# Performance work log

Hardware: AMD Instinct MI355X
Metric: run time of the kernel (lower is better)

Reference implementation:

```python
import jax, jax.numpy as jnp
import numpy as np

D = 16        # d_model
DFF = 128     # ffn hidden
H_NN = 128    # pairwise-MLP hidden
RES = 1.0     # res_ratio (undefined global in source; standard residual)
EPS = 1e-6


def setup_inputs() -> dict:
    key = jax.random.key(0)
    ks = jax.random.split(key, 16)
    B, G, L = 8, 1, 256
    def n(k, shape, s=0.05):
        return jax.random.normal(k, shape, jnp.float32) * s
    return dict(
        x=jax.random.normal(ks[0], (B, G, L, D), jnp.float32),
        mask=jnp.zeros((B, G, L, L), jnp.float32),
        wq=n(ks[1], (D, D)), bq=jnp.zeros((D,), jnp.float32),
        wk=n(ks[2], (D, D)), bk=jnp.zeros((D,), jnp.float32),
        wv=n(ks[3], (D, D)), bv=jnp.zeros((D,), jnp.float32),
        wo=n(ks[4], (D, D)), bo=jnp.zeros((D,), jnp.float32),
        nn_w1=n(ks[5], (2 * D, H_NN)), nn_b1=jnp.zeros((H_NN,), jnp.float32),
        nn_w2=n(ks[6], (H_NN, 1)), nn_b2=jnp.zeros((1,), jnp.float32),
        f1=n(ks[7], (D, DFF)), f1b=jnp.zeros((DFF,), jnp.float32),
        f2=n(ks[8], (DFF, D)), f2b=jnp.zeros((D,), jnp.float32),
        g1=jnp.ones((D,), jnp.float32), be1=jnp.zeros((D,), jnp.float32),
        g2=jnp.ones((D,), jnp.float32), be2=jnp.zeros((D,), jnp.float32),
    )


def _layernorm(x, g, b):
    m = jnp.mean(x, -1, keepdims=True)
    v = jnp.var(x, -1, keepdims=True)
    return (x - m) * jax.lax.rsqrt(v + EPS) * g + b


def reference(x, mask, wq, bq, wk, bk, wv, bv, wo, bo,
              nn_w1, nn_b1, nn_w2, nn_b2,
              f1, f1b, f2, f2b, g1, be1, g2, be2):
    # projections: (B,G,L,D)
    q = x @ wq + bq
    k = x @ wk + bk
    v = x @ wv + bv
    # pairwise relation-network attention.
    # NN(concat([q_i, k_j])) first layer splits as q_i @ W1[:D] + k_j @ W1[D:]
    w1q, w1k = nn_w1[:D], nn_w1[D:]
    w2 = nn_w2[:, 0]
    qa = q @ w1q  # (B,G,L,H)
    kb = k @ w1k
    h1 = jax.nn.relu(qa[:, :, :, None, :] + kb[:, :, None, :, :] + nn_b1)  # (B,G,Lq,Lk,H)
    logits = jnp.einsum('bgijh,h->bgij', h1, w2) + nn_b2[0]
    # make_sym: NN(concat([k_j, q_i])) -> k_j @ W1[:D] + q_i @ W1[D:]
    ka = k @ w1q
    qb = q @ w1k
    h2 = jax.nn.relu(qb[:, :, :, None, :] + ka[:, :, None, :, :] + nn_b1)
    logits = logits + jnp.einsum('bgijh,h->bgij', h2, w2) + nn_b2[0]
    logits = logits + mask * -1e9
    attn = jax.nn.softmax(logits, axis=-1)          # (B,G,Lq,Lk)
    ctx = jnp.einsum('bgij,bgjd->bgid', attn, v)    # (B,G,L,D)
    attn_out = ctx @ wo + bo
    out1 = _layernorm(RES * x + (2.0 - RES) * attn_out, g1, be1)
    ffn = jax.nn.relu(out1 @ f1 + f1b) @ f2 + f2b
    out2 = _layernorm(RES * out1 + (2.0 - RES) * ffn, g2, be2)
    return out2
```

## Files before the change

kernel.cpp:

```cpp
#include <hip/hip_runtime.h>
#include <hip/hip_bf16.h>

typedef __hip_bfloat16 bf16;
typedef float f32x4 __attribute__((ext_vector_type(4)));

constexpr int DIM  = 16;
constexpr int HNN  = 128;
constexpr int SEQ  = 256;
constexpr int BAT  = 8;
constexpr int ROWS = BAT * SEQ;
constexpr int HP   = HNN / 2;
constexpr int QT   = 4;
constexpr int NQT  = ROWS / QT;
constexpr int QHP  = 16;

__device__ __forceinline__ bool is_f32(const void* g1) {
  return ((const unsigned*)g1)[0] == 0x3F800000u;
}
__device__ __forceinline__ float ld(const void* p, long i, bool f32) {
  return f32 ? ((const float*)p)[i]
             : __bfloat162float(((const bf16*)p)[i]);
}

__global__ __launch_bounds__(128) void prep_kernel(
    const void* __restrict__ x,
    const void* __restrict__ wq, const void* __restrict__ bq,
    const void* __restrict__ wk, const void* __restrict__ bk,
    const void* __restrict__ wv, const void* __restrict__ bv,
    const void* __restrict__ nn_w1, const void* __restrict__ nn_b1,
    const void* __restrict__ nn_w2, const void* __restrict__ g1flag,
    float* __restrict__ kkT, float* __restrict__ qq,
    float* __restrict__ vT,  float2* __restrict__ w2p)
{
  const bool f32 = is_f32(g1flag);
  const int row = blockIdx.x;
  const int tid = threadIdx.x;
  __shared__ float xs[DIM], qs[DIM], ks[DIM], vs[DIM];

  if (tid < DIM) xs[tid] = ld(x, (long)row * DIM + tid, f32);
  __syncthreads();

  if (tid < 3 * DIM) {
    const int which = tid >> 4, d = tid & 15;
    const void* w  = (which == 0) ? wq : (which == 1) ? wk : wv;
    const void* bb = (which == 0) ? bq : (which == 1) ? bk : bv;
    float acc = ld(bb, d, f32);
    #pragma unroll
    for (int e = 0; e < DIM; e++) acc += xs[e] * ld(w, e * DIM + d, f32);
    if (which == 0) qs[d] = acc;
    else if (which == 1) ks[d] = acc;
    else vs[d] = acc;
  }
  __syncthreads();

  float qw1q = 0.f, qw1k = 0.f, kw1q = 0.f, kw1k = 0.f;
  #pragma unroll
  for (int d = 0; d < DIM; d++) {
    float a = ld(nn_w1, d * HNN + tid, f32);
    float b = ld(nn_w1, (DIM + d) * HNN + tid, f32);
    qw1q += qs[d] * a;  qw1k += qs[d] * b;
    kw1q += ks[d] * a;  kw1k += ks[d] * b;
  }
  const float b1 = ld(nn_b1, tid, f32);
  const int hp = tid >> 1, half = tid & 1;
  ((float2*)kkT)[((size_t)hp * ROWS + row) * 2 + half] =
      make_float2(kw1k + b1, kw1q + b1);
  ((float2*)qq)[((size_t)row * HP + hp) * 2 + half] =
      make_float2(qw1q, qw1k);
  if (tid < DIM) vT[tid * ROWS + row] = vs[tid];
  if (row == 0 && tid < HP)
    w2p[tid] = make_float2(ld(nn_w2, 2 * tid, f32), ld(nn_w2, 2 * tid + 1, f32));
}

__global__ __launch_bounds__(256) void logits_kernel(
    const f32x4* __restrict__ kkT, const f32x4* __restrict__ qq,
    const float2* __restrict__ w2p, float* __restrict__ part)
{
  const int bid     = blockIdx.x;
  const int qt      = bid & (NQT - 1);
  const int quarter = bid >> 9;
  const int bi = qt >> 6;
  const int i0 = (qt & 63) * QT;
  const int j  = threadIdx.x;
  const int col = bi * SEQ + j;

  const f32x4* kkbase = kkT + (size_t)quarter * QHP * ROWS + col;
  const f32x4* qbase  = qq + (size_t)(bi * SEQ + i0) * HP + quarter * QHP;
  const float2* wbase = w2p + quarter * QHP;

  const f32x4 z = {0.f, 0.f, 0.f, 0.f};
  f32x4 acc0 = z, acc1 = z, acc2 = z, acc3 = z;

  #pragma unroll 4
  for (int m = 0; m < QHP; ++m) {
    const f32x4 kk = kkbase[(size_t)m * ROWS];
    const float2 w = wbase[m];
    const f32x4 w4 = {w.x, w.x, w.y, w.y};
    const f32x4 q0 = qbase[0 * HP + m];
    const f32x4 q1 = qbase[1 * HP + m];
    const f32x4 q2 = qbase[2 * HP + m];
    const f32x4 q3 = qbase[3 * HP + m];
    acc0 = __builtin_elementwise_fma(__builtin_elementwise_max(q0 + kk, z), w4, acc0);
    acc1 = __builtin_elementwise_fma(__builtin_elementwise_max(q1 + kk, z), w4, acc1);
    acc2 = __builtin_elementwise_fma(__builtin_elementwise_max(q2 + kk, z), w4, acc2);
    acc3 = __builtin_elementwise_fma(__builtin_elementwise_max(q3 + kk, z), w4, acc3);
  }

  float* dst = part + ((size_t)quarter * ROWS + (bi * SEQ + i0)) * SEQ + j;
  dst[0 * SEQ] = acc0.x + acc0.y + acc0.z + acc0.w;
  dst[1 * SEQ] = acc1.x + acc1.y + acc1.z + acc1.w;
  dst[2 * SEQ] = acc2.x + acc2.y + acc2.z + acc2.w;
  dst[3 * SEQ] = acc3.x + acc3.y + acc3.z + acc3.w;
}

__global__ __launch_bounds__(256) void tail_kernel(
    const void* __restrict__ x,  const void* __restrict__ mask,
    const void* __restrict__ wo, const void* __restrict__ bo,
    const void* __restrict__ nn_b2,
    const void* __restrict__ f1, const void* __restrict__ f1b,
    const void* __restrict__ f2, const void* __restrict__ f2b,
    const void* __restrict__ g1, const void* __restrict__ be1,
    const void* __restrict__ g2, const void* __restrict__ be2,
    const float* __restrict__ part, const float* __restrict__ vT,
    void* __restrict__ out)
{
  const bool f32 = is_f32(g1);
  const int qidx = blockIdx.x;
  const int bi   = qidx >> 8;
  const int j    = threadIdx.x;
  const int col  = bi * SEQ + j;
  const int lane = j & 63, wvi = j >> 6;

  __shared__ float pb[SEQ];
  __shared__ float vbuf[SEQ][DIM + 1];
  __shared__ float red[2][4];
  __shared__ float cpart[DIM][17];
  __shared__ float ctxs[DIM], rr[DIM], o1[DIM], hid[HNN];

  #pragma unroll
  for (int d = 0; d < DIM; ++d) vbuf[j][d] = vT[d * ROWS + col];

  const float* pp = part + (size_t)qidx * SEQ + j;
  const size_t QS = (size_t)ROWS * SEQ;
  float logit = pp[0] + pp[QS] + pp[2 * QS] + pp[3 * QS]
              + 2.f * ld(nn_b2, 0, f32)
              + ld(mask, (size_t)qidx * SEQ + j, f32) * -1e9f;

  float m = logit;
  #pragma unroll
  for (int off = 32; off > 0; off >>= 1) m = fmaxf(m, __shfl_xor(m, off, 64));
  if (lane == 0) red[0][wvi] = m;
  __syncthreads();
  const float mx = fmaxf(fmaxf(red[0][0], red[0][1]), fmaxf(red[0][2], red[0][3]));
  const float e = __expf(logit - mx);
  pb[j] = e;
  float s = e;
  #pragma unroll
  for (int off = 32; off > 0; off >>= 1) s += __shfl_xor(s, off, 64);
  if (lane == 0) red[1][wvi] = s;
  __syncthreads();
  const float inv = 1.f / (red[1][0] + red[1][1] + red[1][2] + red[1][3]);

  {
    const int d = j & 15, c = j >> 4;
    float sacc = 0.f;
    #pragma unroll
    for (int jj = 0; jj < 16; ++jj)
      sacc += pb[c * 16 + jj] * vbuf[c * 16 + jj][d];
    cpart[d][c] = sacc;
  }
  __syncthreads();
  if (j < DIM) {
    float sc = 0.f;
    #pragma unroll
    for (int c = 0; c < 16; ++c) sc += cpart[j][c];
    ctxs[j] = sc * inv;
  }
  __syncthreads();

  if (j < DIM) {
    float ao = ld(bo, j, f32);
    #pragma unroll
    for (int dd = 0; dd < DIM; ++dd) ao += ctxs[dd] * ld(wo, dd * DIM + j, f32);
    rr[j] = ld(x, (long)qidx * DIM + j, f32) + ao;
  }
  __syncthreads();
  if (j < DIM) {
    float mn = 0.f;
    #pragma unroll
    for (int dd = 0; dd < DIM; ++dd) mn += rr[dd];
    mn *= (1.f / DIM);
    float vv = 0.f;
    #pragma unroll
    for (int dd = 0; dd < DIM; ++dd) { float zz = rr[dd] - mn; vv += zz * zz; }
    vv *= (1.f / DIM);
    o1[j] = (rr[j] - mn) * rsqrtf(vv + 1e-6f) * ld(g1, j, f32) + ld(be1, j, f32);
  }
  __syncthreads();

  if (j < HNN) {
    float a = ld(f1b, j, f32);
    #pragma unroll
    for (int dd = 0; dd < DIM; ++dd) a += o1[dd] * ld(f1, dd * HNN + j, f32);
    hid[j] = fmaxf(a, 0.f);
  }
  __syncthreads();

  {
    const int d = j & 15, c = j >> 4;
    float a = 0.f;
    #pragma unroll
    for (int hh = 0; hh < 8; ++hh) {
      const int h = c * 8 + hh;
      a += hid[h] * ld(f2, h * DIM + d, f32);
    }
    cpart[d][c] = a;
  }
  __syncthreads();
  if (j < DIM) {
    float a = ld(f2b, j, f32);
    #pragma unroll
    for (int c = 0; c < 16; ++c) a += cpart[j][c];
    rr[j] = o1[j] + a;
  }
  __syncthreads();

  if (j < DIM) {
    float mn = 0.f;
    #pragma unroll
    for (int dd = 0; dd < DIM; ++dd) mn += rr[dd];
    mn *= (1.f / DIM);
    float vv = 0.f;
    #pragma unroll
    for (int dd = 0; dd < DIM; ++dd) { float zz = rr[dd] - mn; vv += zz * zz; }
    vv *= (1.f / DIM);
    const float val = (rr[j] - mn) * rsqrtf(vv + 1e-6f) * ld(g2, j, f32)
                    + ld(be2, j, f32);
    const long oidx = (long)qidx * DIM + j;
    if (f32) ((float*)out)[oidx] = val;
    else     ((bf16*)out)[oidx] = __float2bfloat16(val);
  }
}

extern "C" void kernel_launch(void* const* d_in, const int* in_sizes, int n_in,
                              void* d_out, int out_size, void* d_ws, size_t ws_size,
                              hipStream_t stream) {
  const void* x     = d_in[0];
  const void* mask  = d_in[1];
  const void* wq    = d_in[2];
  const void* bq    = d_in[3];
  const void* wk    = d_in[4];
  const void* bk    = d_in[5];
  const void* wv    = d_in[6];
  const void* bv    = d_in[7];
  const void* wo    = d_in[8];
  const void* bo    = d_in[9];
  const void* nn_w1 = d_in[10];
  const void* nn_b1 = d_in[11];
  const void* nn_w2 = d_in[12];
  const void* nn_b2 = d_in[13];
  const void* f1    = d_in[14];
  const void* f1b   = d_in[15];
  const void* f2    = d_in[16];
  const void* f2b   = d_in[17];
  const void* g1    = d_in[18];
  const void* be1   = d_in[19];
  const void* g2    = d_in[20];
  const void* be2   = d_in[21];

  float*  kkT  = (float*)d_ws;
  float*  qq   = kkT + (size_t)HP * ROWS * 4;
  float*  vT   = qq  + (size_t)ROWS * HP * 4;
  float*  part = vT  + (size_t)DIM * ROWS;
  float2* w2p  = (float2*)(part + (size_t)4 * ROWS * SEQ);

  prep_kernel<<<ROWS, 128, 0, stream>>>(x, wq, bq, wk, bk, wv, bv,
                                        nn_w1, nn_b1, nn_w2, g1,
                                        kkT, qq, vT, w2p);
  logits_kernel<<<4 * NQT, 256, 0, stream>>>((const f32x4*)kkT, (const f32x4*)qq,
                                             (const float2*)w2p, part);
  tail_kernel<<<ROWS, 256, 0, stream>>>(x, mask, wo, bo, nn_b2,
                                        f1, f1b, f2, f2b, g1, be1, g2, be2,
                                        part, vT, d_out);
}
```

Before: 126.2 us.

## Fuse three stages into one cooperative kernel with grid-wide syncs

Merges the prep, logits and tail stages into a single cooperative kernel of ROWS blocks, separated by grid.sync, when occupancy allows at least 8 blocks per CU. This removes two kernel launches and their gaps. The logits stage now stages the q vectors and w2 weights in shared memory instead of reading them from global memory each iteration. The tail stage reads V directly from global memory instead of first copying it into shared memory. Grid syncs and the extra fences add their own cost, and a cooperative launch of 2048 blocks depends on every block being resident at once.

```diff
diff --git a/kernel.cpp b/kernel.cpp
--- a/kernel.cpp
+++ b/kernel.cpp
@@ -1,5 +1,8 @@
 #include <hip/hip_runtime.h>
 #include <hip/hip_bf16.h>
+#include <hip/hip_cooperative_groups.h>
+
+namespace cg = cooperative_groups;
 
 typedef __hip_bfloat16 bf16;
 typedef float f32x4 __attribute__((ext_vector_type(4)));
@@ -20,6 +23,222 @@
 __device__ __forceinline__ float ld(const void* p, long i, bool f32) {
   return f32 ? ((const float*)p)[i]
              : __bfloat162float(((const bf16*)p)[i]);
+}
+
+__global__ __launch_bounds__(256, 8) void fused_kernel(
+    const void* __restrict__ x,  const void* __restrict__ mask,
+    const void* __restrict__ wq, const void* __restrict__ bq,
+    const void* __restrict__ wk, const void* __restrict__ bk,
+    const void* __restrict__ wv, const void* __restrict__ bv,
+    const void* __restrict__ wo, const void* __restrict__ bo,
+    const void* __restrict__ nn_w1, const void* __restrict__ nn_b1,
+    const void* __restrict__ nn_w2, const void* __restrict__ nn_b2,
+    const void* __restrict__ f1, const void* __restrict__ f1b,
+    const void* __restrict__ f2, const void* __restrict__ f2b,
+    const void* __restrict__ g1, const void* __restrict__ be1,
+    const void* __restrict__ g2, const void* __restrict__ be2,
+    float* __restrict__ kkT, float* __restrict__ qq,
+    float* __restrict__ vT,  float2* __restrict__ w2p,
+    float* __restrict__ part, void* __restrict__ out)
+{
+  const bool f32 = is_f32(g1);
+  const int t   = threadIdx.x;
+  const int blk = blockIdx.x;
+  cg::grid_group grid = cg::this_grid();
+
+  __shared__ float xs[DIM], qs[DIM], ks[DIM], vs[DIM];
+  __shared__ f32x4 sqq[QT][QHP];
+  __shared__ float2 sw2[QHP];
+  __shared__ float pb[SEQ];
+  __shared__ float red[2][4];
+  __shared__ float cpart[DIM][17];
+  __shared__ float ctxs[DIM], rr[DIM], o1[DIM], hid[HNN];
+
+  {
+    const int row = blk;
+    if (t < DIM) xs[t] = ld(x, (long)row * DIM + t, f32);
+    __syncthreads();
+    if (t < 3 * DIM) {
+      const int which = t >> 4, d = t & 15;
+      const void* w  = (which == 0) ? wq : (which == 1) ? wk : wv;
+      const void* bb = (which == 0) ? bq : (which == 1) ? bk : bv;
+      float acc = ld(bb, d, f32);
+      #pragma unroll
+      for (int e = 0; e < DIM; e++) acc += xs[e] * ld(w, e * DIM + d, f32);
+      if (which == 0) qs[d] = acc;
+      else if (which == 1) ks[d] = acc;
+      else vs[d] = acc;
+    }
+    __syncthreads();
+    if (t < HNN) {
+      float qw1q = 0.f, qw1k = 0.f, kw1q = 0.f, kw1k = 0.f;
+      #pragma unroll
+      for (int d = 0; d < DIM; d++) {
+        float a = ld(nn_w1, d * HNN + t, f32);
+        float b = ld(nn_w1, (DIM + d) * HNN + t, f32);
+        qw1q += qs[d] * a;  qw1k += qs[d] * b;
+        kw1q += ks[d] * a;  kw1k += ks[d] * b;
+      }
+      const float b1 = ld(nn_b1, t, f32);
+      const int hp = t >> 1, half = t & 1;
+      ((float2*)kkT)[((size_t)hp * ROWS + row) * 2 + half] =
+          make_float2(kw1k + b1, kw1q + b1);
+      ((float2*)qq)[((size_t)row * HP + hp) * 2 + half] =
+          make_float2(qw1q, qw1k);
+      if (t < DIM) vT[t * ROWS + row] = vs[t];
+      if (row == 0 && t < HP)
+        w2p[t] = make_float2(ld(nn_w2, 2 * t, f32), ld(nn_w2, 2 * t + 1, f32));
+    }
+    __threadfence();
+  }
+  grid.sync();
+
+  {
+    const int qt      = blk & (NQT - 1);
+    const int quarter = blk >> 9;
+    const int bi = qt >> 6;
+    const int i0 = (qt & 63) * QT;
+    const int j  = t;
+    const int col = bi * SEQ + j;
+    const f32x4* qq4  = (const f32x4*)qq;
+    const f32x4* kk4  = (const f32x4*)kkT;
+
+    if (t < QT * QHP)
+      sqq[t >> 4][t & 15] =
+          qq4[(size_t)(bi * SEQ + i0 + (t >> 4)) * HP + quarter * QHP + (t & 15)];
+    if (t >= 128 && t < 128 + QHP) sw2[t - 128] = w2p[quarter * QHP + (t - 128)];
+    __syncthreads();
+
+    const f32x4* kkbase = kk4 + (size_t)quarter * QHP * ROWS + col;
+    const f32x4 z = {0.f, 0.f, 0.f, 0.f};
+    f32x4 acc0 = z, acc1 = z, acc2 = z, acc3 = z;
+    #pragma unroll 4
+    for (int m = 0; m < QHP; ++m) {
+      const f32x4 kk = kkbase[(size_t)m * ROWS];
+      const float2 w = sw2[m];
+      const f32x4 w4 = {w.x, w.x, w.y, w.y};
+      const f32x4 q0 = sqq[0][m], q1 = sqq[1][m], q2 = sqq[2][m], q3 = sqq[3][m];
+      acc0 = __builtin_elementwise_fma(__builtin_elementwise_max(q0 + kk, z), w4, acc0);
+      acc1 = __builtin_elementwise_fma(__builtin_elementwise_max(q1 + kk, z), w4, acc1);
+      acc2 = __builtin_elementwise_fma(__builtin_elementwise_max(q2 + kk, z), w4, acc2);
+      acc3 = __builtin_elementwise_fma(__builtin_elementwise_max(q3 + kk, z), w4, acc3);
+    }
+    float* dst = part + ((size_t)quarter * ROWS + (bi * SEQ + i0)) * SEQ + j;
+    dst[0 * SEQ] = acc0.x + acc0.y + acc0.z + acc0.w;
+    dst[1 * SEQ] = acc1.x + acc1.y + acc1.z + acc1.w;
+    dst[2 * SEQ] = acc2.x + acc2.y + acc2.z + acc2.w;
+    dst[3 * SEQ] = acc3.x + acc3.y + acc3.z + acc3.w;
+    __threadfence();
+  }
+  grid.sync();
+
+  {
+    const int qidx = blk;
+    const int bi   = qidx >> 8;
+    const int j    = t;
+    const int lane = j & 63, wvi = j >> 6;
+
+    const float* pp = part + (size_t)qidx * SEQ + j;
+    const size_t QS = (size_t)ROWS * SEQ;
+    float logit = pp[0] + pp[QS] + pp[2 * QS] + pp[3 * QS]
+                + 2.f * ld(nn_b2, 0, f32)
+                + ld(mask, (size_t)qidx * SEQ + j, f32) * -1e9f;
+
+    float m = logit;
+    #pragma unroll
+    for (int off = 32; off > 0; off >>= 1) m = fmaxf(m, __shfl_xor(m, off, 64));
+    if (lane == 0) red[0][wvi] = m;
+    __syncthreads();
+    const float mx = fmaxf(fmaxf(red[0][0], red[0][1]), fmaxf(red[0][2], red[0][3]));
+    const float e = __expf(logit - mx);
+    pb[j] = e;
+    float s = e;
+    #pragma unroll
+    for (int off = 32; off > 0; off >>= 1) s += __shfl_xor(s, off, 64);
+    if (lane == 0) red[1][wvi] = s;
+    __syncthreads();
+    const float inv = 1.f / (red[1][0] + red[1][1] + red[1][2] + red[1][3]);
+
+    {
+      const int d = j & 15, c = j >> 4;
+      const float* vrow = vT + d * ROWS + bi * SEQ + c * 16;
+      float sacc = 0.f;
+      #pragma unroll
+      for (int jj = 0; jj < 16; ++jj) sacc += pb[c * 16 + jj] * vrow[jj];
+      cpart[d][c] = sacc;
+    }
+    __syncthreads();
+    if (j < DIM) {
+      float sc = 0.f;
+      #pragma unroll
+      for (int c = 0; c < 16; ++c) sc += cpart[j][c];
+      ctxs[j] = sc * inv;
+    }
+    __syncthreads();
+
+    if (j < DIM) {
+      float ao = ld(bo, j, f32);
+      #pragma unroll
+      for (int dd = 0; dd < DIM; ++dd) ao += ctxs[dd] * ld(wo, dd * DIM + j, f32);
+      rr[j] = ld(x, (long)qidx * DIM + j, f32) + ao;
+    }
+    __syncthreads();
+    if (j < DIM) {
+      float mn = 0.f;
+      #pragma unroll
+      for (int dd = 0; dd < DIM; ++dd) mn += rr[dd];
+      mn *= (1.f / DIM);
+      float vv = 0.f;
+      #pragma unroll
+      for (int dd = 0; dd < DIM; ++dd) { float zz = rr[dd] - mn; vv += zz * zz; }
+      vv *= (1.f / DIM);
+      o1[j] = (rr[j] - mn) * rsqrtf(vv + 1e-6f) * ld(g1, j, f32) + ld(be1, j, f32);
+    }
+    __syncthreads();
+
+    if (j < HNN) {
+      float a = ld(f1b, j, f32);
+      #pragma unroll
+      for (int dd = 0; dd < DIM; ++dd) a += o1[dd] * ld(f1, dd * HNN + j, f32);
+      hid[j] = fmaxf(a, 0.f);
+    }
+    __syncthreads();
+
+    {
+      const int d = j & 15, c = j >> 4;
+      float a = 0.f;
+      #pragma unroll
+      for (int hh = 0; hh < 8; ++hh) {
+        const int h = c * 8 + hh;
+        a += hid[h] * ld(f2, h * DIM + d, f32);
+      }
+      cpart[d][c] = a;
+    }
+    __syncthreads();
+    if (j < DIM) {
+      float a = ld(f2b, j, f32);
+      #pragma unroll
+      for (int c = 0; c < 16; ++c) a += cpart[j][c];
+      rr[j] = o1[j] + a;
+    }
+    __syncthreads();
+
+    if (j < DIM) {
+      float mn = 0.f;
+      #pragma unroll
+      for (int dd = 0; dd < DIM; ++dd) mn += rr[dd];
+      mn *= (1.f / DIM);
+      float vv = 0.f;
+      #pragma unroll
+      for (int dd = 0; dd < DIM; ++dd) { float zz = rr[dd] - mn; vv += zz * zz; }
+      vv *= (1.f / DIM);
+      const float val = (rr[j] - mn) * rsqrtf(vv + 1e-6f) * ld(g2, j, f32)
+                      + ld(be2, j, f32);
+      const long oidx = (long)qidx * DIM + j;
+      if (f32) ((float*)out)[oidx] = val;
+      else     ((bf16*)out)[oidx] = __float2bfloat16(val);
+    }
+  }
 }
 
 __global__ __launch_bounds__(128) void prep_kernel(
@@ -39,7 +258,6 @@
 
   if (tid < DIM) xs[tid] = ld(x, (long)row * DIM + tid, f32);
   __syncthreads();
-
   if (tid < 3 * DIM) {
     const int which = tid >> 4, d = tid & 15;
     const void* w  = (which == 0) ? wq : (which == 1) ? wk : wv;
@@ -52,7 +270,6 @@
     else vs[d] = acc;
   }
   __syncthreads();
-
   float qw1q = 0.f, qw1k = 0.f, kw1q = 0.f, kw1k = 0.f;
   #pragma unroll
   for (int d = 0; d < DIM; d++) {
@@ -84,28 +301,28 @@
   const int j  = threadIdx.x;
   const int col = bi * SEQ + j;
 
+  __shared__ f32x4 sqq[QT][QHP];
+  __shared__ float2 sw2[QHP];
+  if (j < QT * QHP)
+    sqq[j >> 4][j & 15] =
+        qq[(size_t)(bi * SEQ + i0 + (j >> 4)) * HP + quarter * QHP + (j & 15)];
+  if (j >= 128 && j < 128 + QHP) sw2[j - 128] = w2p[quarter * QHP + (j - 128)];
+  __syncthreads();
+
   const f32x4* kkbase = kkT + (size_t)quarter * QHP * ROWS + col;
-  const f32x4* qbase  = qq + (size_t)(bi * SEQ + i0) * HP + quarter * QHP;
-  const float2* wbase = w2p + quarter * QHP;
-
   const f32x4 z = {0.f, 0.f, 0.f, 0.f};
   f32x4 acc0 = z, acc1 = z, acc2 = z, acc3 = z;
-
   #pragma unroll 4
   for (int m = 0; m < QHP; ++m) {
     const f32x4 kk = kkbase[(size_t)m * ROWS];
-    const float2 w = wbase[m];
+    const float2 w = sw2[m];
     const f32x4 w4 = {w.x, w.x, w.y, w.y};
-    const f32x4 q0 = qbase[0 * HP + m];
-    const f32x4 q1 = qbase[1 * HP + m];
-    const f32x4 q2 = qbase[2 * HP + m];
-    const f32x4 q3 = qbase[3 * HP + m];
+    const f32x4 q0 = sqq[0][m], q1 = sqq[1][m], q2 = sqq[2][m], q3 = sqq[3][m];
     acc0 = __builtin_elementwise_fma(__builtin_elementwise_max(q0 + kk, z), w4, acc0);
     acc1 = __builtin_elementwise_fma(__builtin_elementwise_max(q1 + kk, z), w4, acc1);
     acc2 = __builtin_elementwise_fma(__builtin_elementwise_max(q2 + kk, z), w4, acc2);
     acc3 = __builtin_elementwise_fma(__builtin_elementwise_max(q3 + kk, z), w4, acc3);
   }
-
   float* dst = part + ((size_t)quarter * ROWS + (bi * SEQ + i0)) * SEQ + j;
   dst[0 * SEQ] = acc0.x + acc0.y + acc0.z + acc0.w;
   dst[1 * SEQ] = acc1.x + acc1.y + acc1.z + acc1.w;
@@ -128,17 +345,12 @@
   const int qidx = blockIdx.x;
   const int bi   = qidx >> 8;
   const int j    = threadIdx.x;
-  const int col  = bi * SEQ + j;
   const int lane = j & 63, wvi = j >> 6;
 
   __shared__ float pb[SEQ];
-  __shared__ float vbuf[SEQ][DIM + 1];
   __shared__ float red[2][4];
   __shared__ float cpart[DIM][17];
   __shared__ float ctxs[DIM], rr[DIM], o1[DIM], hid[HNN];
-
-  #pragma unroll
-  for (int d = 0; d < DIM; ++d) vbuf[j][d] = vT[d * ROWS + col];
 
   const float* pp = part + (size_t)qidx * SEQ + j;
   const size_t QS = (size_t)ROWS * SEQ;
@@ -163,10 +375,10 @@
 
   {
     const int d = j & 15, c = j >> 4;
+    const float* vrow = vT + d * ROWS + bi * SEQ + c * 16;
     float sacc = 0.f;
     #pragma unroll
-    for (int jj = 0; jj < 16; ++jj)
-      sacc += pb[c * 16 + jj] * vbuf[c * 16 + jj][d];
+    for (int jj = 0; jj < 16; ++jj) sacc += pb[c * 16 + jj] * vrow[jj];
     cpart[d][c] = sacc;
   }
   __syncthreads();
@@ -177,7 +389,6 @@
     ctxs[j] = sc * inv;
   }
   __syncthreads();
-
   if (j < DIM) {
     float ao = ld(bo, j, f32);
     #pragma unroll
@@ -197,7 +408,6 @@
     o1[j] = (rr[j] - mn) * rsqrtf(vv + 1e-6f) * ld(g1, j, f32) + ld(be1, j, f32);
   }
   __syncthreads();
-
   if (j < HNN) {
     float a = ld(f1b, j, f32);
     #pragma unroll
@@ -205,7 +415,6 @@
     hid[j] = fmaxf(a, 0.f);
   }
   __syncthreads();
-
   {
     const int d = j & 15, c = j >> 4;
     float a = 0.f;
@@ -224,7 +433,6 @@
     rr[j] = o1[j] + a;
   }
   __syncthreads();
-
   if (j < DIM) {
     float mn = 0.f;
     #pragma unroll
@@ -273,13 +481,28 @@
   float*  vT   = qq  + (size_t)ROWS * HP * 4;
   float*  part = vT  + (size_t)DIM * ROWS;
   float2* w2p  = (float2*)(part + (size_t)4 * ROWS * SEQ);
-
-  prep_kernel<<<ROWS, 128, 0, stream>>>(x, wq, bq, wk, bk, wv, bv,
-                                        nn_w1, nn_b1, nn_w2, g1,
-                                        kkT, qq, vT, w2p);
-  logits_kernel<<<4 * NQT, 256, 0, stream>>>((const f32x4*)kkT, (const f32x4*)qq,
-                                             (const float2*)w2p, part);
-  tail_kernel<<<ROWS, 256, 0, stream>>>(x, mask, wo, bo, nn_b2,
-                                        f1, f1b, f2, f2b, g1, be1, g2, be2,
-                                        part, vT, d_out);
-}
+  void*   outp = d_out;
+
+  int nb = 0;
+  hipError_t oe = hipOccupancyMaxActiveBlocksPerMultiprocessor(
+      &nb, fused_kernel, 256, 0);
+  if (oe == hipSuccess && nb >= 8) {
+    void* kp[] = {
+      (void*)&x,  (void*)&mask, (void*)&wq, (void*)&bq, (void*)&wk, (void*)&bk,
+      (void*)&wv, (void*)&bv,   (void*)&wo, (void*)&bo, (void*)&nn_w1,
+      (void*)&nn_b1, (void*)&nn_w2, (void*)&nn_b2, (void*)&f1, (void*)&f1b,
+      (void*)&f2, (void*)&f2b, (void*)&g1, (void*)&be1, (void*)&g2, (void*)&be2,
+      (void*)&kkT, (void*)&qq, (void*)&vT, (void*)&w2p, (void*)&part, (void*)&outp
+    };
+    hipLaunchCooperativeKernel(fused_kernel, dim3(ROWS), dim3(256), kp, 0, stream);
+  } else {
+    prep_kernel<<<ROWS, 128, 0, stream>>>(x, wq, bq, wk, bk, wv, bv,
+                                          nn_w1, nn_b1, nn_w2, g1,
+                                          kkT, qq, vT, w2p);
+    logits_kernel<<<4 * NQT, 256, 0, stream>>>((const f32x4*)kkT, (const f32x4*)qq,
+                                               (const float2*)w2p, part);
+    tail_kernel<<<ROWS, 256, 0, stream>>>(x, mask, wo, bo, nn_b2,
+                                          f1, f1b, f2, f2b, g1, be1, g2, be2,
+                                          part, vT, d_out);
+  }
+}
```

Result: slower. 129.9 us (+2.9%).

## Split hidden dim in halves, stage q/w2 in LDS, read V directly in tail

Applied to the files above, without the earlier changes.

The logits kernel now splits the pairwise-MLP hidden dimension into two halves instead of four. Each block handles twice as many hidden units, which halves the partial-logit buffer the tail kernel must write and read. Per-block q and w2 values are staged in shared memory instead of being loaded from global memory every iteration. The tail kernel drops the shared V buffer and reads vT straight from global in the context reduction. The trade-off is half as many logits blocks, each with a longer loop, and uncached, less coalesced V reads.

```diff
diff --git a/kernel.cpp b/kernel.cpp
--- a/kernel.cpp
+++ b/kernel.cpp
@@ -12,7 +12,7 @@
 constexpr int HP   = HNN / 2;
 constexpr int QT   = 4;
 constexpr int NQT  = ROWS / QT;
-constexpr int QHP  = 16;
+constexpr int HHP  = 32;
 
 __device__ __forceinline__ bool is_f32(const void* g1) {
   return ((const unsigned*)g1)[0] == 0x3F800000u;
@@ -76,37 +76,41 @@
     const f32x4* __restrict__ kkT, const f32x4* __restrict__ qq,
     const float2* __restrict__ w2p, float* __restrict__ part)
 {
-  const int bid     = blockIdx.x;
-  const int qt      = bid & (NQT - 1);
-  const int quarter = bid >> 9;
+  const int bid  = blockIdx.x;
+  const int qt   = bid & (NQT - 1);
+  const int half = bid >> 9;
   const int bi = qt >> 6;
   const int i0 = (qt & 63) * QT;
   const int j  = threadIdx.x;
   const int col = bi * SEQ + j;
 
-  const f32x4* kkbase = kkT + (size_t)quarter * QHP * ROWS + col;
-  const f32x4* qbase  = qq + (size_t)(bi * SEQ + i0) * HP + quarter * QHP;
-  const float2* wbase = w2p + quarter * QHP;
-
+  __shared__ f32x4 sqq[QT][HHP];
+  __shared__ float2 sw2[HHP];
+
+  if (j < QT * HHP) {
+    const int ii = j >> 5, m = j & 31;
+    sqq[ii][m] = qq[(size_t)(bi * SEQ + i0 + ii) * HP + half * HHP + m];
+  }
+  if (j >= 128 && j < 128 + HHP) sw2[j - 128] = w2p[half * HHP + (j - 128)];
+  __syncthreads();
+
+  const f32x4* kkbase = kkT + (size_t)half * HHP * ROWS + col;
   const f32x4 z = {0.f, 0.f, 0.f, 0.f};
   f32x4 acc0 = z, acc1 = z, acc2 = z, acc3 = z;
 
   #pragma unroll 4
-  for (int m = 0; m < QHP; ++m) {
+  for (int m = 0; m < HHP; ++m) {
     const f32x4 kk = kkbase[(size_t)m * ROWS];
-    const float2 w = wbase[m];
+    const float2 w = sw2[m];
     const f32x4 w4 = {w.x, w.x, w.y, w.y};
-    const f32x4 q0 = qbase[0 * HP + m];
-    const f32x4 q1 = qbase[1 * HP + m];
-    const f32x4 q2 = qbase[2 * HP + m];
-    const f32x4 q3 = qbase[3 * HP + m];
+    const f32x4 q0 = sqq[0][m], q1 = sqq[1][m], q2 = sqq[2][m], q3 = sqq[3][m];
     acc0 = __builtin_elementwise_fma(__builtin_elementwise_max(q0 + kk, z), w4, acc0);
     acc1 = __builtin_elementwise_fma(__builtin_elementwise_max(q1 + kk, z), w4, acc1);
     acc2 = __builtin_elementwise_fma(__builtin_elementwise_max(q2 + kk, z), w4, acc2);
     acc3 = __builtin_elementwise_fma(__builtin_elementwise_max(q3 + kk, z), w4, acc3);
   }
 
-  float* dst = part + ((size_t)quarter * ROWS + (bi * SEQ + i0)) * SEQ + j;
+  float* dst = part + ((size_t)half * ROWS + (bi * SEQ + i0)) * SEQ + j;
   dst[0 * SEQ] = acc0.x + acc0.y + acc0.z + acc0.w;
   dst[1 * SEQ] = acc1.x + acc1.y + acc1.z + acc1.w;
   dst[2 * SEQ] = acc2.x + acc2.y + acc2.z + acc2.w;
@@ -128,21 +132,16 @@
   const int qidx = blockIdx.x;
   const int bi   = qidx >> 8;
   const int j    = threadIdx.x;
-  const int col  = bi * SEQ + j;
   const int lane = j & 63, wvi = j >> 6;
 
   __shared__ float pb[SEQ];
-  __shared__ float vbuf[SEQ][DIM + 1];
   __shared__ float red[2][4];
   __shared__ float cpart[DIM][17];
   __shared__ float ctxs[DIM], rr[DIM], o1[DIM], hid[HNN];
 
-  #pragma unroll
-  for (int d = 0; d < DIM; ++d) vbuf[j][d] = vT[d * ROWS + col];
-
   const float* pp = part + (size_t)qidx * SEQ + j;
   const size_t QS = (size_t)ROWS * SEQ;
-  float logit = pp[0] + pp[QS] + pp[2 * QS] + pp[3 * QS]
+  float logit = pp[0] + pp[QS]
               + 2.f * ld(nn_b2, 0, f32)
               + ld(mask, (size_t)qidx * SEQ + j, f32) * -1e9f;
 
@@ -163,10 +162,10 @@
 
   {
     const int d = j & 15, c = j >> 4;
+    const float* vrow = vT + d * ROWS + bi * SEQ + c * 16;
     float sacc = 0.f;
     #pragma unroll
-    for (int jj = 0; jj < 16; ++jj)
-      sacc += pb[c * 16 + jj] * vbuf[c * 16 + jj][d];
+    for (int jj = 0; jj < 16; ++jj) sacc += pb[c * 16 + jj] * vrow[jj];
     cpart[d][c] = sacc;
   }
   __syncthreads();
@@ -177,7 +176,6 @@
     ctxs[j] = sc * inv;
   }
   __syncthreads();
-
   if (j < DIM) {
     float ao = ld(bo, j, f32);
     #pragma unroll
@@ -197,7 +195,6 @@
     o1[j] = (rr[j] - mn) * rsqrtf(vv + 1e-6f) * ld(g1, j, f32) + ld(be1, j, f32);
   }
   __syncthreads();
-
   if (j < HNN) {
     float a = ld(f1b, j, f32);
     #pragma unroll
@@ -205,7 +202,6 @@
     hid[j] = fmaxf(a, 0.f);
   }
   __syncthreads();
-
   {
     const int d = j & 15, c = j >> 4;
     float a = 0.f;
@@ -224,7 +220,6 @@
     rr[j] = o1[j] + a;
   }
   __syncthreads();
-
   if (j < DIM) {
     float mn = 0.f;
     #pragma unroll
@@ -272,12 +267,12 @@
   float*  qq   = kkT + (size_t)HP * ROWS * 4;
   float*  vT   = qq  + (size_t)ROWS * HP * 4;
   float*  part = vT  + (size_t)DIM * ROWS;
-  float2* w2p  = (float2*)(part + (size_t)4 * ROWS * SEQ);
+  float2* w2p  = (float2*)(part + (size_t)2 * ROWS * SEQ);
 
   prep_kernel<<<ROWS, 128, 0, stream>>>(x, wq, bq, wk, bk, wv, bv,
                                         nn_w1, nn_b1, nn_w2, g1,
                                         kkT, qq, vT, w2p);
-  logits_kernel<<<4 * NQT, 256, 0, stream>>>((const f32x4*)kkT, (const f32x4*)qq,
+  logits_kernel<<<2 * NQT, 256, 0, stream>>>((const f32x4*)kkT, (const f32x4*)qq,
                                              (const float2*)w2p, part);
   tail_kernel<<<ROWS, 256, 0, stream>>>(x, mask, wo, bo, nn_b2,
                                         f1, f1b, f2, f2b, g1, be1, g2, be2,
```

Result: no change. 127.1 us (+0.7%).
